# Performance work log

Measured on AMD Instinct MI355X. Metric: run time of the kernel, lower is better.

## Reference

```python
import jax, jax.numpy as jnp
import numpy as np

INPUT_SIZE = 128
HID = 64
B, T = 256, 2048


def _uniform(key, shape, scale):
    return jax.random.uniform(key, shape, jnp.float32, -scale, scale)


def setup_inputs() -> dict:
    key = jax.random.key(0)
    ks = jax.random.split(key, 11)
    s = 1.0 / np.sqrt(HID)  # torch LSTM/Linear init scale
    x = jax.random.normal(ks[0], (B, T, INPUT_SIZE), jnp.float32)
    return {
        "x": x,
        "W_ih1": _uniform(ks[1], (4 * HID, INPUT_SIZE), s),
        "W_hh1": _uniform(ks[2], (4 * HID, HID), s),
        "b_ih1": _uniform(ks[3], (4 * HID,), s),
        "b_hh1": _uniform(ks[4], (4 * HID,), s),
        "W_ih2": _uniform(ks[5], (4 * HID, HID), s),
        "W_hh2": _uniform(ks[6], (4 * HID, HID), s),
        "b_ih2": _uniform(ks[7], (4 * HID,), s),
        "b_hh2": _uniform(ks[8], (4 * HID,), s),
        "W_out": _uniform(ks[9], (1, HID), s),
        "b_out": _uniform(ks[10], (1,), s),
    }


def _lstm_layer(x, W_ih, W_hh, b_ih, b_hh):
    # x: [B, T, F] -> h_seq: [B, T, H]. Torch gate order: i, f, g, o.
    Bd = x.shape[0]
    H = W_hh.shape[1]
    # Precompute input projection for all timesteps (one big GEMM).
    xp = jnp.einsum("btf,gf->btg", x, W_ih) + b_ih + b_hh  # [B, T, 4H]

    def step(carry, xt):
        h, c = carry
        gates = xt + h @ W_hh.T  # [B, 4H]
        i, f, g, o = jnp.split(gates, 4, axis=-1)
        i = jax.nn.sigmoid(i)
        f = jax.nn.sigmoid(f)
        g = jnp.tanh(g)
        o = jax.nn.sigmoid(o)
        c = f * c + i * g
        h = o * jnp.tanh(c)
        return (h, c), h

    h0 = jnp.zeros((Bd, H), x.dtype)
    c0 = jnp.zeros((Bd, H), x.dtype)
    _, hs = jax.lax.scan(step, (h0, c0), jnp.swapaxes(xp, 0, 1))  # [T, B, H]
    return jnp.swapaxes(hs, 0, 1)


def reference(x, W_ih1, W_hh1, b_ih1, b_hh1, W_ih2, W_hh2, b_ih2, b_hh2, W_out, b_out):
    h1 = _lstm_layer(x, W_ih1, W_hh1, b_ih1, b_hh1)   # dropout is identity in eval
    h2 = _lstm_layer(h1, W_ih2, W_hh2, b_ih2, b_hh2)
    r = jnp.einsum("bth,oh->bto", h2, W_out) + b_out   # [B, T, 1]
    return jnp.clip(r, 0.0, 1.0)
```

## Files before the change

### kernel.cpp

```cpp
#include <hip/hip_runtime.h>
#include <hip/hip_bf16.h>

#define Bsz  256
#define Tlen 2048
#define IN   128
#define H    64


typedef float v2f __attribute__((ext_vector_type(2)));

static __device__ __forceinline__ float bfbits2f(unsigned int u16) {
    union { unsigned int i; float f; } v; v.i = u16 << 16; return v.f;
}
static __device__ __forceinline__ v2f unpack_v2(unsigned int u) {
    union { unsigned int i; float f; } a, b;
    a.i = u << 16; b.i = u & 0xFFFF0000u;
    v2f r; r.x = a.f; r.y = b.f; return r;
}
static __device__ __forceinline__ v2f mkv2(float a, float b) { v2f r; r.x = a; r.y = b; return r; }
static __device__ __forceinline__ v2f fma2(v2f a, v2f b, v2f c) {
    return __builtin_elementwise_fma(a, b, c);
}

static __device__ __forceinline__ int detect_bf16(const unsigned int* w) {
    int ok = 1;
#pragma unroll
    for (int i = 0; i < 32; ++i) {
        unsigned int u = w[i];
        float lo = bfbits2f(u & 0xFFFFu);
        float hi = bfbits2f(u >> 16);
        ok &= (fabsf(lo) <= 0.1251f) & (fabsf(hi) <= 0.1251f);
    }
    return ok;
}

template<bool BF>
static __device__ __forceinline__ float ld1(const void* p, size_t i) {
    if (BF) return bfbits2f(((const unsigned short*)p)[i]);
    else    return ((const float*)p)[i];
}

template<bool BF, int N>
static __device__ __forceinline__ void load_slice(v2f* dst, const void* src, size_t off) {
    if (BF) {
        const uint4* p = (const uint4*)((const unsigned short*)src + off);
#pragma unroll
        for (int i = 0; i < N / 8; ++i) {
            uint4 qd = p[i];
            dst[4*i+0] = unpack_v2(qd.x);
            dst[4*i+1] = unpack_v2(qd.y);
            dst[4*i+2] = unpack_v2(qd.z);
            dst[4*i+3] = unpack_v2(qd.w);
        }
    } else {
        const float4* p = (const float4*)((const float*)src + off);
#pragma unroll
        for (int i = 0; i < N / 4; ++i) {
            float4 qd = p[i];
            dst[2*i+0] = mkv2(qd.x, qd.y);
            dst[2*i+1] = mkv2(qd.z, qd.w);
        }
    }
}

static __device__ __forceinline__ float fast_rcp(float x) { return __builtin_amdgcn_rcpf(x); }
static __device__ __forceinline__ float sigm(float x)  { return fast_rcp(1.0f + __expf(-x)); }
static __device__ __forceinline__ float tanh_f(float x){
    float e = __expf(2.0f * x);
    return fmaf(-2.0f, fast_rcp(e + 1.0f), 1.0f);
}

template<int CTRL>
static __device__ __forceinline__ float dpp_sum_step(float x) {
    union { float f; int i; } u, v;
    u.f = x;
    v.i = __builtin_amdgcn_update_dpp(0, u.i, CTRL, 0xF, 0xF, true);
    return x + v.f;
}
static __device__ __forceinline__ float dpp8_allsum(float x) {
    x = dpp_sum_step<0xB1>(x);
    x = dpp_sum_step<0x4E>(x);
    x = dpp_sum_step<0x141>(x);
    return x;
}

struct alignas(16) SharedMem {
    float h1[2][H];
    float h2[2][H];
    float hist[H][H + 1];
};

template<bool BF>
static __device__ void lstm_core(SharedMem* sm,
    const void* x,    const void* Wih1, const void* Whh1,
    const void* bih1, const void* bhh1, const void* Wih2,
    const void* Whh2, const void* bih2, const void* bhh2,
    const void* Wout, const void* bout, void* outp,
    int b, int tid)
{
    const int q = tid & 7;
    const int j = tid >> 3;

    v2f wx1[4][8], wh1[4][4], wx2[4][4], wh2[4][4];
    float bias1[4], bias2[4];
#pragma unroll
    for (int a = 0; a < 4; ++a) {
        const int g = a * H + j;
        load_slice<BF, 16>(wx1[a], Wih1, (size_t)g * IN + q * 16);
        load_slice<BF, 8 >(wh1[a], Whh1, (size_t)g * H  + q * 8);
        load_slice<BF, 8 >(wx2[a], Wih2, (size_t)g * H  + q * 8);
        load_slice<BF, 8 >(wh2[a], Whh2, (size_t)g * H  + q * 8);
        bias1[a] = ld1<BF>(bih1, g) + ld1<BF>(bhh1, g);
        bias2[a] = ld1<BF>(bih2, g) + ld1<BF>(bhh2, g);
    }
    float wout_r[8];
#pragma unroll
    for (int i = 0; i < 8; ++i) wout_r[i] = ld1<BF>(Wout, q * 8 + i);
    const float boutv = ld1<BF>(bout, 0);

    if (tid < H) sm->h2[1][tid] = 0.f;

    const unsigned short* xb_b = (const unsigned short*)x + (size_t)b * Tlen * IN + q * 16;
    const float*          xb_f = (const float*)x          + (size_t)b * Tlen * IN + q * 16;

    uint4  rb0, rb1;
    float4 rf0, rf1, rf2, rf3;
    v2f xc[8];

    auto load_x = [&](int t) {
        if (BF) {
            const uint4* p = (const uint4*)(xb_b + (size_t)t * IN);
            rb0 = p[0]; rb1 = p[1];
        } else {
            const float4* p = (const float4*)(xb_f + (size_t)t * IN);
            rf0 = p[0]; rf1 = p[1]; rf2 = p[2]; rf3 = p[3];
        }
    };
    auto unpack_x = [&]() {
        if (BF) {
            xc[0] = unpack_v2(rb0.x); xc[1] = unpack_v2(rb0.y);
            xc[2] = unpack_v2(rb0.z); xc[3] = unpack_v2(rb0.w);
            xc[4] = unpack_v2(rb1.x); xc[5] = unpack_v2(rb1.y);
            xc[6] = unpack_v2(rb1.z); xc[7] = unpack_v2(rb1.w);
        } else {
            xc[0] = mkv2(rf0.x, rf0.y); xc[1] = mkv2(rf0.z, rf0.w);
            xc[2] = mkv2(rf1.x, rf1.y); xc[3] = mkv2(rf1.z, rf1.w);
            xc[4] = mkv2(rf2.x, rf2.y); xc[5] = mkv2(rf2.z, rf2.w);
            xc[6] = mkv2(rf3.x, rf3.y); xc[7] = mkv2(rf3.z, rf3.w);
        }
    };

    float c1, c2 = 0.f;

    load_x(0); unpack_x();
    load_x(1);
    {
        v2f a0 = mkv2(0.f, 0.f), a1 = a0, a2 = a0, a3 = a0;
#pragma unroll
        for (int p = 0; p < 8; ++p) {
            a0 = fma2(wx1[0][p], xc[p], a0);
            a1 = fma2(wx1[1][p], xc[p], a1);
            a2 = fma2(wx1[2][p], xc[p], a2);
            a3 = fma2(wx1[3][p], xc[p], a3);
        }
        float r0 = dpp8_allsum(a0.x + a0.y) + bias1[0];
        float r1 = dpp8_allsum(a1.x + a1.y) + bias1[1];
        float r2 = dpp8_allsum(a2.x + a2.y) + bias1[2];
        float r3 = dpp8_allsum(a3.x + a3.y) + bias1[3];
        float i_ = sigm(r0), f_ = sigm(r1), g_ = tanh_f(r2), o_ = sigm(r3);
        (void)f_;
        c1 = i_ * g_;
        float h1n = o_ * tanh_f(c1);
        if (q == 0) sm->h1[0][j] = h1n;
    }
    __syncthreads();

    for (int t = 0; t < Tlen; ++t) {
        const float4* h1p = (const float4*)&sm->h1[t & 1][q * 8];
        const float4* h2p = (const float4*)&sm->h2[(t + 1) & 1][q * 8];
        float4 nA = h1p[0], nB = h1p[1];
        float4 oA = h2p[0], oB = h2p[1];

        const bool havex = (t + 1 < Tlen);
        if (havex) unpack_x();
        if (t + 2 < Tlen) load_x(t + 2);

        v2f a0 = mkv2(0.f, 0.f), a1 = a0, a2 = a0, a3 = a0;
        if (havex) {
#pragma unroll
            for (int p = 0; p < 8; ++p) {
                a0 = fma2(wx1[0][p], xc[p], a0);
                a1 = fma2(wx1[1][p], xc[p], a1);
                a2 = fma2(wx1[2][p], xc[p], a2);
                a3 = fma2(wx1[3][p], xc[p], a3);
            }
        }

        v2f nv[4] = { mkv2(nA.x,nA.y), mkv2(nA.z,nA.w), mkv2(nB.x,nB.y), mkv2(nB.z,nB.w) };
        v2f ov[4] = { mkv2(oA.x,oA.y), mkv2(oA.z,oA.w), mkv2(oB.x,oB.y), mkv2(oB.z,oB.w) };

        v2f e0 = mkv2(0.f, 0.f), e1 = e0, e2 = e0, e3 = e0;
#pragma unroll
        for (int p = 0; p < 4; ++p) {
            e0 = fma2(wx2[0][p], nv[p], e0);
            e1 = fma2(wx2[1][p], nv[p], e1);
            e2 = fma2(wx2[2][p], nv[p], e2);
            e3 = fma2(wx2[3][p], nv[p], e3);
        }
#pragma unroll
        for (int p = 0; p < 4; ++p) {
            e0 = fma2(wh2[0][p], ov[p], e0);
            e1 = fma2(wh2[1][p], ov[p], e1);
            e2 = fma2(wh2[2][p], ov[p], e2);
            e3 = fma2(wh2[3][p], ov[p], e3);
        }

        if (havex) {
#pragma unroll
            for (int p = 0; p < 4; ++p) {
                a0 = fma2(wh1[0][p], nv[p], a0);
                a1 = fma2(wh1[1][p], nv[p], a1);
                a2 = fma2(wh1[2][p], nv[p], a2);
                a3 = fma2(wh1[3][p], nv[p], a3);
            }
        }

        {
            float s0 = dpp8_allsum(e0.x + e0.y) + bias2[0];
            float s1 = dpp8_allsum(e1.x + e1.y) + bias2[1];
            float s2 = dpp8_allsum(e2.x + e2.y) + bias2[2];
            float s3 = dpp8_allsum(e3.x + e3.y) + bias2[3];
            float i_ = sigm(s0), f_ = sigm(s1), g_ = tanh_f(s2), o_ = sigm(s3);
            c2 = fmaf(f_, c2, i_ * g_);
            float h2n = o_ * tanh_f(c2);
            if (q == 0) {
                sm->h2[t & 1][j] = h2n;
                sm->hist[j][t & 63] = h2n;
            }
        }

        if (havex) {
            float r0 = dpp8_allsum(a0.x + a0.y) + bias1[0];
            float r1 = dpp8_allsum(a1.x + a1.y) + bias1[1];
            float r2 = dpp8_allsum(a2.x + a2.y) + bias1[2];
            float r3 = dpp8_allsum(a3.x + a3.y) + bias1[3];
            float i_ = sigm(r0), f_ = sigm(r1), g_ = tanh_f(r2), o_ = sigm(r3);
            c1 = fmaf(f_, c1, i_ * g_);
            float h1n = o_ * tanh_f(c1);
            if (q == 0) sm->h1[(t + 1) & 1][j] = h1n;
        }

        if ((t & 63) == 63) {
            __syncthreads();
            const int tt = j;
            float s = 0.f;
#pragma unroll
            for (int i = 0; i < 8; ++i)
                s = fmaf(wout_r[i], sm->hist[q * 8 + i][tt], s);
            s = dpp8_allsum(s);
            if (q == 0) {
                s += boutv;
                s = fminf(fmaxf(s, 0.f), 1.f);
                const size_t oi = (size_t)b * Tlen + (t - 63) + tt;
                if (BF) ((__hip_bfloat16*)outp)[oi] = __float2bfloat16(s);
                else    ((float*)outp)[oi] = s;
            }
        }

        __syncthreads();
    }
}

__global__ __launch_bounds__(512, 2)
void lstm2_fused(const void* __restrict__ x,    const void* __restrict__ Wih1,
                 const void* __restrict__ Whh1, const void* __restrict__ bih1,
                 const void* __restrict__ bhh1, const void* __restrict__ Wih2,
                 const void* __restrict__ Whh2, const void* __restrict__ bih2,
                 const void* __restrict__ bhh2, const void* __restrict__ Wout,
                 const void* __restrict__ bout, void* __restrict__ outp)
{
    __shared__ SharedMem sm;
    __shared__ int mode_bf;
    const int tid = threadIdx.x;
    if (tid == 0) mode_bf = detect_bf16((const unsigned int*)Wih1);
    __syncthreads();

    if (mode_bf)
        lstm_core<true >(&sm, x, Wih1, Whh1, bih1, bhh1, Wih2, Whh2, bih2, bhh2,
                         Wout, bout, outp, blockIdx.x, tid);
    else
        lstm_core<false>(&sm, x, Wih1, Whh1, bih1, bhh1, Wih2, Whh2, bih2, bhh2,
                         Wout, bout, outp, blockIdx.x, tid);
}

extern "C" void kernel_launch(void* const* d_in, const int* in_sizes, int n_in,
                              void* d_out, int out_size, void* d_ws, size_t ws_size,
                              hipStream_t stream)
{
    (void)in_sizes; (void)n_in; (void)d_ws; (void)ws_size; (void)out_size;
    lstm2_fused<<<dim3(Bsz), dim3(512), 0, stream>>>(
        d_in[0], d_in[1], d_in[2], d_in[3], d_in[4], d_in[5],
        d_in[6], d_in[7], d_in[8], d_in[9], d_in[10], d_out);
}
```

Measured before the change: 2.167 ms.

## Use 4 lanes per hidden unit with per-lane gate activation and DPP broadcast

Halves the block to 256 threads so each hidden unit's dot products are split across 4 lanes instead of 8, doubling per-thread weight slices and shortening the DPP reduction to two steps. Each lane then applies a single activation for its own gate (tanh expressed as a scaled sigmoid for the g gate), and the four gate values are shared via quad DPP broadcasts, replacing four transcendental evaluations per lane with one. This cuts block-wide barrier cost and redundant activation work, at the expense of longer serial FMA chains per step and higher register pressure per thread.

After: 3.113 ms. 1.44x slower.

```diff
diff --git a/kernel.cpp b/kernel.cpp
--- a/kernel.cpp
+++ b/kernel.cpp
@@ -5,6 +5,8 @@
 #define Tlen 2048
 #define IN   128
 #define H    64
+#define XS   (IN/4)
+#define HS   (H/4)
 
 
 typedef float v2f __attribute__((ext_vector_type(2)));
@@ -64,7 +66,6 @@
 }
 
 static __device__ __forceinline__ float fast_rcp(float x) { return __builtin_amdgcn_rcpf(x); }
-static __device__ __forceinline__ float sigm(float x)  { return fast_rcp(1.0f + __expf(-x)); }
 static __device__ __forceinline__ float tanh_f(float x){
     float e = __expf(2.0f * x);
     return fmaf(-2.0f, fast_rcp(e + 1.0f), 1.0f);
@@ -77,11 +78,32 @@
     v.i = __builtin_amdgcn_update_dpp(0, u.i, CTRL, 0xF, 0xF, true);
     return x + v.f;
 }
-static __device__ __forceinline__ float dpp8_allsum(float x) {
+static __device__ __forceinline__ float dpp4_allsum(float x) {
     x = dpp_sum_step<0xB1>(x);
     x = dpp_sum_step<0x4E>(x);
-    x = dpp_sum_step<0x141>(x);
     return x;
+}
+template<int CTRL>
+static __device__ __forceinline__ float qbcast(float x) {
+    union { float f; int i; } u, v;
+    u.f = x;
+    v.i = __builtin_amdgcn_update_dpp(0, u.i, CTRL, 0xF, 0xF, true);
+    return v.f;
+}
+
+static __device__ __forceinline__ float lstm_combine(
+    float r0, float r1, float r2, float r3,
+    int q, float bown, float sc1, float sc2, float off, float& c)
+{
+    float own = (q == 0 ? r0 : q == 1 ? r1 : q == 2 ? r2 : r3) + bown;
+    float s   = fast_rcp(1.0f + __expf(-(own * sc1)));
+    float act = fmaf(s, sc2, off);
+    float i_ = qbcast<0x00>(act);
+    float f_ = qbcast<0x55>(act);
+    float g_ = qbcast<0xAA>(act);
+    float o_ = qbcast<0xFF>(act);
+    c = fmaf(f_, c, i_ * g_);
+    return o_ * tanh_f(c);
 }
 
 struct alignas(16) SharedMem {
@@ -98,88 +120,95 @@
     const void* Wout, const void* bout, void* outp,
     int b, int tid)
 {
-    const int q = tid & 7;
-    const int j = tid >> 3;
-
-    v2f wx1[4][8], wh1[4][4], wx2[4][4], wh2[4][4];
-    float bias1[4], bias2[4];
+    const int q = tid & 3;
+    const int j = tid >> 2;
+
+    v2f wx1[4][XS/2], wh1[4][HS/2], wx2[4][HS/2], wh2[4][HS/2];
 #pragma unroll
     for (int a = 0; a < 4; ++a) {
         const int g = a * H + j;
-        load_slice<BF, 16>(wx1[a], Wih1, (size_t)g * IN + q * 16);
-        load_slice<BF, 8 >(wh1[a], Whh1, (size_t)g * H  + q * 8);
-        load_slice<BF, 8 >(wx2[a], Wih2, (size_t)g * H  + q * 8);
-        load_slice<BF, 8 >(wh2[a], Whh2, (size_t)g * H  + q * 8);
-        bias1[a] = ld1<BF>(bih1, g) + ld1<BF>(bhh1, g);
-        bias2[a] = ld1<BF>(bih2, g) + ld1<BF>(bhh2, g);
-    }
-    float wout_r[8];
-#pragma unroll
-    for (int i = 0; i < 8; ++i) wout_r[i] = ld1<BF>(Wout, q * 8 + i);
+        load_slice<BF, XS>(wx1[a], Wih1, (size_t)g * IN + q * XS);
+        load_slice<BF, HS>(wh1[a], Whh1, (size_t)g * H  + q * HS);
+        load_slice<BF, HS>(wx2[a], Wih2, (size_t)g * H  + q * HS);
+        load_slice<BF, HS>(wh2[a], Whh2, (size_t)g * H  + q * HS);
+    }
+    const int gq = q * H + j;
+    const float bown1 = ld1<BF>(bih1, gq) + ld1<BF>(bhh1, gq);
+    const float bown2 = ld1<BF>(bih2, gq) + ld1<BF>(bhh2, gq);
+    const float sc1 = (q == 2) ? 2.0f : 1.0f;
+    const float sc2 = (q == 2) ? 2.0f : 1.0f;
+    const float off = (q == 2) ? -1.0f : 0.0f;
+
+    float wout_r[HS];
+#pragma unroll
+    for (int i = 0; i < HS; ++i) wout_r[i] = ld1<BF>(Wout, q * HS + i);
     const float boutv = ld1<BF>(bout, 0);
 
     if (tid < H) sm->h2[1][tid] = 0.f;
 
-    const unsigned short* xb_b = (const unsigned short*)x + (size_t)b * Tlen * IN + q * 16;
-    const float*          xb_f = (const float*)x          + (size_t)b * Tlen * IN + q * 16;
-
-    uint4  rb0, rb1;
-    float4 rf0, rf1, rf2, rf3;
-    v2f xc[8];
+    const unsigned short* xb_b = (const unsigned short*)x + (size_t)b * Tlen * IN + q * XS;
+    const float*          xb_f = (const float*)x          + (size_t)b * Tlen * IN + q * XS;
+
+    uint4  rb[4];
+    float4 rf[8];
+    v2f xc[XS/2];
 
     auto load_x = [&](int t) {
         if (BF) {
             const uint4* p = (const uint4*)(xb_b + (size_t)t * IN);
-            rb0 = p[0]; rb1 = p[1];
+#pragma unroll
+            for (int i = 0; i < 4; ++i) rb[i] = p[i];
         } else {
             const float4* p = (const float4*)(xb_f + (size_t)t * IN);
-            rf0 = p[0]; rf1 = p[1]; rf2 = p[2]; rf3 = p[3];
+#pragma unroll
+            for (int i = 0; i < 8; ++i) rf[i] = p[i];
         }
     };
     auto unpack_x = [&]() {
         if (BF) {
-            xc[0] = unpack_v2(rb0.x); xc[1] = unpack_v2(rb0.y);
-            xc[2] = unpack_v2(rb0.z); xc[3] = unpack_v2(rb0.w);
-            xc[4] = unpack_v2(rb1.x); xc[5] = unpack_v2(rb1.y);
-            xc[6] = unpack_v2(rb1.z); xc[7] = unpack_v2(rb1.w);
+#pragma unroll
+            for (int i = 0; i < 4; ++i) {
+                xc[4*i+0] = unpack_v2(rb[i].x);
+                xc[4*i+1] = unpack_v2(rb[i].y);
+                xc[4*i+2] = unpack_v2(rb[i].z);
+                xc[4*i+3] = unpack_v2(rb[i].w);
+            }
         } else {
-            xc[0] = mkv2(rf0.x, rf0.y); xc[1] = mkv2(rf0.z, rf0.w);
-            xc[2] = mkv2(rf1.x, rf1.y); xc[3] = mkv2(rf1.z, rf1.w);
-            xc[4] = mkv2(rf2.x, rf2.y); xc[5] = mkv2(rf2.z, rf2.w);
-            xc[6] = mkv2(rf3.x, rf3.y); xc[7] = mkv2(rf3.z, rf3.w);
+#pragma unroll
+            for (int i = 0; i < 8; ++i) {
+                xc[2*i+0] = mkv2(rf[i].x, rf[i].y);
+                xc[2*i+1] = mkv2(rf[i].z, rf[i].w);
+            }
         }
     };
 
-    float c1, c2 = 0.f;
+    float c1 = 0.f, c2 = 0.f;
 
     load_x(0); unpack_x();
     load_x(1);
     {
         v2f a0 = mkv2(0.f, 0.f), a1 = a0, a2 = a0, a3 = a0;
 #pragma unroll
-        for (int p = 0; p < 8; ++p) {
+        for (int p = 0; p < XS/2; ++p) {
             a0 = fma2(wx1[0][p], xc[p], a0);
             a1 = fma2(wx1[1][p], xc[p], a1);
             a2 = fma2(wx1[2][p], xc[p], a2);
             a3 = fma2(wx1[3][p], xc[p], a3);
         }
-        float r0 = dpp8_allsum(a0.x + a0.y) + bias1[0];
-        float r1 = dpp8_allsum(a1.x + a1.y) + bias1[1];
-        float r2 = dpp8_allsum(a2.x + a2.y) + bias1[2];
-        float r3 = dpp8_allsum(a3.x + a3.y) + bias1[3];
-        float i_ = sigm(r0), f_ = sigm(r1), g_ = tanh_f(r2), o_ = sigm(r3);
-        (void)f_;
-        c1 = i_ * g_;
-        float h1n = o_ * tanh_f(c1);
+        float r0 = dpp4_allsum(a0.x + a0.y);
+        float r1 = dpp4_allsum(a1.x + a1.y);
+        float r2 = dpp4_allsum(a2.x + a2.y);
+        float r3 = dpp4_allsum(a3.x + a3.y);
+        float h1n = lstm_combine(r0, r1, r2, r3, q, bown1, sc1, sc2, off, c1);
         if (q == 0) sm->h1[0][j] = h1n;
     }
     __syncthreads();
 
     for (int t = 0; t < Tlen; ++t) {
-        const float4* h1p = (const float4*)&sm->h1[t & 1][q * 8];
-        const float4* h2p = (const float4*)&sm->h2[(t + 1) & 1][q * 8];
-        float4 nA = h1p[0], nB = h1p[1];
-        float4 oA = h2p[0], oB = h2p[1];
+        const float4* h1p = (const float4*)&sm->h1[t & 1][q * HS];
+        const float4* h2p = (const float4*)&sm->h2[(t + 1) & 1][q * HS];
+        float4 nA = h1p[0], nB = h1p[1], nC = h1p[2], nD = h1p[3];
+        float4 oA = h2p[0], oB = h2p[1], oC = h2p[2], oD = h2p[3];
 
         const bool havex = (t + 1 < Tlen);
         if (havex) unpack_x();
@@ -188,7 +217,7 @@
         v2f a0 = mkv2(0.f, 0.f), a1 = a0, a2 = a0, a3 = a0;
         if (havex) {
 #pragma unroll
-            for (int p = 0; p < 8; ++p) {
+            for (int p = 0; p < XS/2; ++p) {
                 a0 = fma2(wx1[0][p], xc[p], a0);
                 a1 = fma2(wx1[1][p], xc[p], a1);
                 a2 = fma2(wx1[2][p], xc[p], a2);
@@ -196,19 +225,21 @@
             }
         }
 
-        v2f nv[4] = { mkv2(nA.x,nA.y), mkv2(nA.z,nA.w), mkv2(nB.x,nB.y), mkv2(nB.z,nB.w) };
-        v2f ov[4] = { mkv2(oA.x,oA.y), mkv2(oA.z,oA.w), mkv2(oB.x,oB.y), mkv2(oB.z,oB.w) };
+        v2f nv[HS/2] = { mkv2(nA.x,nA.y), mkv2(nA.z,nA.w), mkv2(nB.x,nB.y), mkv2(nB.z,nB.w),
+                         mkv2(nC.x,nC.y), mkv2(nC.z,nC.w), mkv2(nD.x,nD.y), mkv2(nD.z,nD.w) };
+        v2f ov[HS/2] = { mkv2(oA.x,oA.y), mkv2(oA.z,oA.w), mkv2(oB.x,oB.y), mkv2(oB.z,oB.w),
+                         mkv2(oC.x,oC.y), mkv2(oC.z,oC.w), mkv2(oD.x,oD.y), mkv2(oD.z,oD.w) };
 
         v2f e0 = mkv2(0.f, 0.f), e1 = e0, e2 = e0, e3 = e0;
 #pragma unroll
-        for (int p = 0; p < 4; ++p) {
+        for (int p = 0; p < HS/2; ++p) {
             e0 = fma2(wx2[0][p], nv[p], e0);
             e1 = fma2(wx2[1][p], nv[p], e1);
             e2 = fma2(wx2[2][p], nv[p], e2);
             e3 = fma2(wx2[3][p], nv[p], e3);
         }
 #pragma unroll
-        for (int p = 0; p < 4; ++p) {
+        for (int p = 0; p < HS/2; ++p) {
             e0 = fma2(wh2[0][p], ov[p], e0);
             e1 = fma2(wh2[1][p], ov[p], e1);
             e2 = fma2(wh2[2][p], ov[p], e2);
@@ -217,7 +248,7 @@
 
         if (havex) {
 #pragma unroll
-            for (int p = 0; p < 4; ++p) {
+            for (int p = 0; p < HS/2; ++p) {
                 a0 = fma2(wh1[0][p], nv[p], a0);
                 a1 = fma2(wh1[1][p], nv[p], a1);
                 a2 = fma2(wh1[2][p], nv[p], a2);
@@ -226,13 +257,11 @@
         }
 
         {
-            float s0 = dpp8_allsum(e0.x + e0.y) + bias2[0];
-            float s1 = dpp8_allsum(e1.x + e1.y) + bias2[1];
-            float s2 = dpp8_allsum(e2.x + e2.y) + bias2[2];
-            float s3 = dpp8_allsum(e3.x + e3.y) + bias2[3];
-            float i_ = sigm(s0), f_ = sigm(s1), g_ = tanh_f(s2), o_ = sigm(s3);
-            c2 = fmaf(f_, c2, i_ * g_);
-            float h2n = o_ * tanh_f(c2);
+            float s0 = dpp4_allsum(e0.x + e0.y);
+            float s1 = dpp4_allsum(e1.x + e1.y);
+            float s2 = dpp4_allsum(e2.x + e2.y);
+            float s3 = dpp4_allsum(e3.x + e3.y);
+            float h2n = lstm_combine(s0, s1, s2, s3, q, bown2, sc1, sc2, off, c2);
             if (q == 0) {
                 sm->h2[t & 1][j] = h2n;
                 sm->hist[j][t & 63] = h2n;
@@ -240,13 +269,11 @@
         }
 
         if (havex) {
-            float r0 = dpp8_allsum(a0.x + a0.y) + bias1[0];
-            float r1 = dpp8_allsum(a1.x + a1.y) + bias1[1];
-            float r2 = dpp8_allsum(a2.x + a2.y) + bias1[2];
-            float r3 = dpp8_allsum(a3.x + a3.y) + bias1[3];
-            float i_ = sigm(r0), f_ = sigm(r1), g_ = tanh_f(r2), o_ = sigm(r3);
-            c1 = fmaf(f_, c1, i_ * g_);
-            float h1n = o_ * tanh_f(c1);
+            float r0 = dpp4_allsum(a0.x + a0.y);
+            float r1 = dpp4_allsum(a1.x + a1.y);
+            float r2 = dpp4_allsum(a2.x + a2.y);
+            float r3 = dpp4_allsum(a3.x + a3.y);
+            float h1n = lstm_combine(r0, r1, r2, r3, q, bown1, sc1, sc2, off, c1);
             if (q == 0) sm->h1[(t + 1) & 1][j] = h1n;
         }
 
@@ -255,9 +282,9 @@
             const int tt = j;
             float s = 0.f;
 #pragma unroll
-            for (int i = 0; i < 8; ++i)
-                s = fmaf(wout_r[i], sm->hist[q * 8 + i][tt], s);
-            s = dpp8_allsum(s);
+            for (int i = 0; i < HS; ++i)
+                s = fmaf(wout_r[i], sm->hist[q * HS + i][tt], s);
+            s = dpp4_allsum(s);
             if (q == 0) {
                 s += boutv;
                 s = fminf(fmaxf(s, 0.f), 1.f);
@@ -271,7 +298,7 @@
     }
 }
 
-__global__ __launch_bounds__(512, 2)
+__global__ __launch_bounds__(256, 1)
 void lstm2_fused(const void* __restrict__ x,    const void* __restrict__ Wih1,
                  const void* __restrict__ Whh1, const void* __restrict__ bih1,
                  const void* __restrict__ bhh1, const void* __restrict__ Wih2,
@@ -298,7 +325,7 @@
                               hipStream_t stream)
 {
     (void)in_sizes; (void)n_in; (void)d_ws; (void)ws_size; (void)out_size;
-    lstm2_fused<<<dim3(Bsz), dim3(512), 0, stream>>>(
+    lstm2_fused<<<dim3(Bsz), dim3(256), 0, stream>>>(
         d_in[0], d_in[1], d_in[2], d_in[3], d_in[4], d_in[5],
         d_in[6], d_in[7], d_in[8], d_in[9], d_in[10], d_out);
 }
```
